# Performance work log

Hardware: AMD Instinct MI355X
Metric: run time of the kernel (lower is better)

The kernel has to match this reference:

```python
import jax, jax.numpy as jnp
import numpy as np
from jax.ops import segment_sum

N_NODES = 50000
N_EDGES = 800000
IN_DIM, HID_DIM, OUT_DIM = 128, 128, 64
N_GRAPHS = 64


def setup_inputs() -> dict:
    key = jax.random.key(0)
    ks = jax.random.split(key, 8)
    x = jax.random.normal(ks[0], (N_NODES, IN_DIM), dtype=jnp.float32)
    edge_index = jax.random.randint(ks[1], (2, N_EDGES), 0, N_NODES, dtype=jnp.int64)
    batch = jnp.sort(jax.random.randint(ks[2], (N_NODES,), 0, N_GRAPHS, dtype=jnp.int64))
    # Glorot-ish init for GCNConv linear weights, zero bias (PyG default)
    W1 = jax.random.normal(ks[3], (IN_DIM, HID_DIM), dtype=jnp.float32) / np.sqrt(IN_DIM)
    b1 = jnp.zeros((HID_DIM,), dtype=jnp.float32)
    W2 = jax.random.normal(ks[4], (HID_DIM, OUT_DIM), dtype=jnp.float32) / np.sqrt(HID_DIM)
    b2 = jnp.zeros((OUT_DIM,), dtype=jnp.float32)
    return {"x": x, "W1": W1, "b1": b1, "W2": W2, "b2": b2,
            "edge_index": edge_index, "batch": batch, "num_graphs": N_GRAPHS}


def _gcn_conv(h, W, b, src, dst, deg_inv_sqrt, n_nodes):
    # h: [N, Fin] -> [N, Fout]; GCNConv: D^{-1/2}(A+I)D^{-1/2} (h W) + b
    hw = h @ W                                   # [N, Fout]
    norm = deg_inv_sqrt[src] * deg_inv_sqrt[dst] # [E]
    msg = hw[src] * norm[:, None]                # [E, Fout] (gather)
    agg = segment_sum(msg, dst, num_segments=n_nodes)  # scatter-add
    # self-loop contribution: norm_ii = deg_inv_sqrt[i]^2
    agg = agg + hw * (deg_inv_sqrt * deg_inv_sqrt)[:, None]
    return agg + b


def reference(x, W1, b1, W2, b2, edge_index, batch, num_graphs):
    n_nodes = x.shape[0]
    src, dst = edge_index[0], edge_index[1]
    # degree of A + I (self-loops added, as in PyG GCNConv default)
    deg = segment_sum(jnp.ones_like(dst, dtype=x.dtype), dst,
                      num_segments=n_nodes) + 1.0
    deg_inv_sqrt = jax.lax.rsqrt(deg)

    h = jax.nn.relu(_gcn_conv(x, W1, b1, src, dst, deg_inv_sqrt, n_nodes))
    h = jax.nn.relu(_gcn_conv(h, W2, b2, src, dst, deg_inv_sqrt, n_nodes))

    # global_mean_pool over batch ids
    sums = segment_sum(h, batch, num_segments=num_graphs)          # [G, Fout]
    counts = segment_sum(jnp.ones((n_nodes,), dtype=h.dtype), batch,
                         num_segments=num_graphs)                  # [G]
    return sums / jnp.maximum(counts, 1.0)[:, None]
```

## Files before the change

kernel.cpp:

```cpp
#include <hip/hip_runtime.h>

typedef float f4 __attribute__((ext_vector_type(4)));
typedef float f2 __attribute__((ext_vector_type(2)));
typedef short s8 __attribute__((ext_vector_type(8)));

union FU { unsigned u[4]; s8 s; };

__device__ __forceinline__ unsigned cvtpk(float lo, float hi){
  unsigned r;
  asm("v_cvt_pk_bf16_f32 %0, %1, %2" : "=v"(r) : "v"(lo), "v"(hi));
  return r;
}

__device__ __forceinline__ float bflo(unsigned v){ return __uint_as_float(v << 16); }
__device__ __forceinline__ float bfhi(unsigned v){ return __uint_as_float(v & 0xFFFF0000u); }

__device__ __forceinline__ int ld_idx(const void* p, int i, int is64){
  if (is64) return (int)((const long long*)p)[i];
  return ((const int*)p)[i];
}

__device__ __forceinline__ int detect64(const unsigned* __restrict__ e_raw, int e){
  int lane = threadIdx.x & 63;
  int lim = (e < 1024) ? e : 1024;
  int nz = 0;
  for (int i = lane; i < lim; i += 64) nz |= (e_raw[2*i + 1] != 0u);
  return (__ballot(nz != 0) == 0ull) ? 1 : 0;
}

template<int NC, int BIN>
__device__ __forceinline__ void gemm_body(const void* __restrict__ Xv,
                                          const float* __restrict__ W,
                                          unsigned short* __restrict__ Yb,
                                          int n, int blk, char* Alds){
  constexpr int NCF = NC/16;
  constexpr int WPC = 8/NCF;
  constexpr int RT  = 8/WPC;
  const int tid  = threadIdx.x;
  const int wave = tid >> 6, lane = tid & 63;
  const int rb = blk * 128;

  const int cbase = (wave % NCF) * 16;
  const int rt0   = (wave / NCF) * RT;
  const int col   = cbase + (lane & 15);
  const int kr0   = (lane >> 4) * 8;
  FU bu[4];
#pragma unroll
  for (int ks = 0; ks < 4; ++ks){
    float wv[8];
#pragma unroll
    for (int j = 0; j < 8; ++j) wv[j] = W[(size_t)(ks*32 + kr0 + j)*NC + col];
#pragma unroll
    for (int q = 0; q < 4; ++q) bu[ks].u[q] = cvtpk(wv[2*q], wv[2*q+1]);
  }

  for (int i = tid; i < 128*32; i += 512){
    int row = i >> 5, kq = i & 31;
    int rsrc = rb + row; if (rsrc >= n) rsrc = n - 1;
    uint2 dw;
    if (BIN){
      dw = ((const uint2*)Xv)[(size_t)rsrc*32 + kq];
    } else {
      f4 xv = ((const f4*)Xv)[(size_t)rsrc*32 + kq];
      dw = make_uint2(cvtpk(xv[0], xv[1]), cvtpk(xv[2], xv[3]));
    }
    int byte = (row*256 + kq*8) ^ ((row & 7) << 4);
    *reinterpret_cast<uint2*>(Alds + byte) = dw;
  }
  __syncthreads();

  f4 acc[RT];
#pragma unroll
  for (int rt = 0; rt < RT; ++rt) acc[rt] = 0.0f;

#pragma unroll
  for (int rt = 0; rt < RT; ++rt){
    const int arow = (rt0 + rt)*16 + (lane & 15);
#pragma unroll
    for (int ks = 0; ks < 4; ++ks){
      int kb = ks*32 + kr0;
      int byte = (arow*256 + kb*2) ^ ((arow & 7) << 4);
      s8 a = *reinterpret_cast<const s8*>(Alds + byte);
      acc[rt] = __builtin_amdgcn_mfma_f32_16x16x32_bf16(a, bu[ks].s, acc[rt], 0, 0, 0);
    }
  }

#pragma unroll
  for (int rt = 0; rt < RT; ++rt){
    int rowb = rb + (rt0 + rt)*16 + 4*(lane >> 4);
#pragma unroll
    for (int r = 0; r < 4; ++r){
      int row = rowb + r;
      if (row < n) Yb[(size_t)row*NC + col] = (unsigned short)cvtpk(acc[rt][r], acc[rt][r]);
    }
  }
}

template<int NC, int BIN>
__global__ __launch_bounds__(512) void gemm_k(const void* __restrict__ X,
                                              const float* __restrict__ W,
                                              unsigned short* __restrict__ Yb, int n){
  __shared__ int4 AldsV[2048];
  gemm_body<NC, BIN>(X, W, Yb, n, blockIdx.x, (char*)AldsV);
}

__global__ __launch_bounds__(512) void fused1_k(const float* __restrict__ X,
                                                const float* __restrict__ W1,
                                                unsigned short* __restrict__ Yb,
                                                const void* __restrict__ eidx,
                                                const void* __restrict__ batchp,
                                                int* __restrict__ counts,
                                                int* __restrict__ batch32,
                                                int n, int e, int GB, int CB){
  __shared__ int4 AldsV[2048];
  __shared__ int hist[512];
  int blk = blockIdx.x;
  if (blk < GB){
    gemm_body<128, 0>(X, W1, Yb, n, blk, (char*)AldsV);
    return;
  }
  blk -= GB;
  const int NBK = (n + 127) >> 7;
  for (int i = threadIdx.x; i < NBK; i += 512) hist[i] = 0;
  __syncthreads();
  int is64 = detect64((const unsigned*)eidx, e);
  int CHK = (e + CB - 1) / CB;
  int beg = blk*CHK, end = min(e, beg + CHK);
  for (int i = beg + (int)threadIdx.x; i < end; i += 512){
    int d = ld_idx(eidx, e + i, is64);
    atomicAdd(&hist[d >> 7], 1);
  }
  __syncthreads();
  for (int i = threadIdx.x; i < NBK; i += 512) counts[i*CB + blk] = hist[i];
  for (int i = blk*512 + (int)threadIdx.x; i < n; i += CB*512)
    batch32[i] = ld_idx(batchp, i, is64);
}

__global__ void scanA_k(const int* __restrict__ counts, int* __restrict__ base,
                        int* __restrict__ bsum, int L){
  __shared__ int sh[256];
  int tid = threadIdx.x;
  int i = blockIdx.x*256 + tid;
  int v = (i < L) ? counts[i] : 0;
  sh[tid] = v; __syncthreads();
  for (int off = 1; off < 256; off <<= 1){
    int t = (tid >= off) ? sh[tid - off] : 0;
    __syncthreads();
    sh[tid] += t;
    __syncthreads();
  }
  if (i < L) base[i] = sh[tid] - v;
  if (tid == 255) bsum[blockIdx.x] = sh[255];
}

__global__ __launch_bounds__(512) void scanB2_k(int* __restrict__ bsum, int nb,
                                                int* __restrict__ rowptr,
                                                float* __restrict__ outsum,
                                                int totalOut, int n, int e){
  __shared__ int sh[512];
  int tid = threadIdx.x;
  int v = (tid < nb) ? bsum[tid] : 0;
  sh[tid] = v; __syncthreads();
  for (int off = 1; off < 512; off <<= 1){
    int t = (tid >= off) ? sh[tid - off] : 0;
    __syncthreads();
    sh[tid] += t;
    __syncthreads();
  }
  if (tid < nb) bsum[tid] = sh[tid] - v;
  if (tid == nb - 1) bsum[nb] = sh[tid];
  if (tid == 0) rowptr[n] = e;
  for (int k = tid; k < totalOut; k += 512) outsum[k] = 0.0f;
}

__global__ __launch_bounds__(512) void scat_k(const void* __restrict__ eidx,
                                              const int* __restrict__ base,
                                              const int* __restrict__ bsum,
                                              int* __restrict__ packed,
                                              int n, int e, int CB){
  __shared__ int cur[512];
  int blk = blockIdx.x, tid = threadIdx.x;
  const int NBK = (n + 127) >> 7;
  for (int i = tid; i < NBK; i += 512) cur[i] = bsum[i] + base[i*CB + blk];
  __syncthreads();
  int is64 = detect64((const unsigned*)eidx, e);
  int CHK = (e + CB - 1) / CB;
  int beg = blk*CHK, end = min(e, beg + CHK);
  for (int i = beg + tid; i < end; i += 512){
    int s = ld_idx(eidx, i, is64);
    int d = ld_idx(eidx, e + i, is64);
    int pos = atomicAdd(&cur[d >> 7], 1);
    packed[pos] = s | ((d & 127) << 16);
  }
}

#define CSR_CAP 6144
__global__ __launch_bounds__(256) void csr_k(const int* __restrict__ packed,
                                             const int* __restrict__ bsum,
                                             int* __restrict__ esrcS,
                                             int* __restrict__ rowptr,
                                             float* __restrict__ dinv, int n){
  __shared__ int vals[CSR_CAP];
  __shared__ int hist[128], off[128], cur[128];
  int b = blockIdx.x, tid = threadIdx.x;
  int sbeg = bsum[b], send = bsum[b + 1];
  int m = send - sbeg;
  int mL = min(m, CSR_CAP);
  for (int i = tid; i < mL; i += 256) vals[i] = packed[sbeg + i];
  if (tid < 128) hist[tid] = 0;
  __syncthreads();
  for (int i = tid; i < m; i += 256){
    int v = (i < CSR_CAP) ? vals[i] : packed[sbeg + i];
    atomicAdd(&hist[(v >> 16) & 127], 1);
  }
  __syncthreads();
  if (tid < 128) off[tid] = hist[tid];
  __syncthreads();
  for (int o = 1; o < 128; o <<= 1){
    int v = 0;
    if (tid < 128 && tid >= o) v = off[tid - o];
    __syncthreads();
    if (tid < 128) off[tid] += v;
    __syncthreads();
  }
  if (tid < 128){
    int ex = off[tid] - hist[tid];
    cur[tid] = ex;
    int node = b*128 + tid;
    if (node < n){
      rowptr[node] = sbeg + ex;
      dinv[node] = rsqrtf((float)hist[tid] + 1.0f);
    }
  }
  __syncthreads();
  for (int i = tid; i < m; i += 256){
    int v = (i < CSR_CAP) ? vals[i] : packed[sbeg + i];
    int pos = atomicAdd(&cur[(v >> 16) & 127], 1);
    esrcS[sbeg + pos] = v & 0xFFFF;
  }
}

template<int NC, int OB>
__global__ __launch_bounds__(256) void agg_k(const unsigned short* __restrict__ HWb,
                                             const float* __restrict__ dinv,
                                             const int* __restrict__ rowptr,
                                             const int* __restrict__ esrcS,
                                             const float* __restrict__ bias,
                                             void* __restrict__ Hout, int n){
  int wid  = (blockIdx.x*256 + threadIdx.x) >> 6;
  int lane = threadIdx.x & 63;
  if (wid >= n) return;
  wid = __builtin_amdgcn_readfirstlane(wid);
  float di = dinv[wid];
  float di2 = di * di;
  int beg = __builtin_amdgcn_readfirstlane(rowptr[wid]);
  int end = __builtin_amdgcn_readfirstlane(rowptr[wid + 1]);
  if (NC == 128){
    unsigned sv = ((const unsigned*)(HWb + (size_t)wid*128))[lane];
    float a0 = bflo(sv) * di2, a1 = bfhi(sv) * di2;
    int j = beg;
    for (; j + 16 <= end; j += 16){
      int s[16]; float dv[16]; unsigned v[16];
#pragma unroll
      for (int t = 0; t < 16; ++t) s[t] = esrcS[j + t];
#pragma unroll
      for (int t = 0; t < 16; ++t){
        dv[t] = dinv[s[t]];
        v[t] = ((const unsigned*)(HWb + (size_t)s[t]*128))[lane];
      }
#pragma unroll
      for (int t = 0; t < 16; ++t){
        float wt = dv[t] * di;
        a0 += bflo(v[t]) * wt;
        a1 += bfhi(v[t]) * wt;
      }
    }
    for (; j + 4 <= end; j += 4){
      int s[4]; float dv[4]; unsigned v[4];
#pragma unroll
      for (int t = 0; t < 4; ++t) s[t] = esrcS[j + t];
#pragma unroll
      for (int t = 0; t < 4; ++t){
        dv[t] = dinv[s[t]];
        v[t] = ((const unsigned*)(HWb + (size_t)s[t]*128))[lane];
      }
#pragma unroll
      for (int t = 0; t < 4; ++t){
        float wt = dv[t] * di;
        a0 += bflo(v[t]) * wt;
        a1 += bfhi(v[t]) * wt;
      }
    }
    for (; j < end; ++j){
      int s = esrcS[j];
      float wt = dinv[s] * di;
      unsigned v = ((const unsigned*)(HWb + (size_t)s*128))[lane];
      a0 += bflo(v) * wt;
      a1 += bfhi(v) * wt;
    }
    f2 bb = ((const f2*)bias)[lane];
    a0 = fmaxf(a0 + bb[0], 0.0f);
    a1 = fmaxf(a1 + bb[1], 0.0f);
    if (OB){
      ((unsigned*)Hout)[(size_t)wid*64 + lane] = cvtpk(a0, a1);
    } else {
      f2 r; r[0] = a0; r[1] = a1;
      ((f2*)Hout)[(size_t)wid*64 + lane] = r;
    }
  } else {
    float acc = bflo((unsigned)HWb[(size_t)wid*64 + lane]) * di2;
    int j = beg;
    for (; j + 16 <= end; j += 16){
      int s[16]; float dv[16]; unsigned v[16];
#pragma unroll
      for (int t = 0; t < 16; ++t) s[t] = esrcS[j + t];
#pragma unroll
      for (int t = 0; t < 16; ++t){
        dv[t] = dinv[s[t]];
        v[t] = (unsigned)HWb[(size_t)s[t]*64 + lane];
      }
#pragma unroll
      for (int t = 0; t < 16; ++t) acc += bflo(v[t]) * (dv[t] * di);
    }
    for (; j + 4 <= end; j += 4){
      int s[4]; float dv[4]; unsigned v[4];
#pragma unroll
      for (int t = 0; t < 4; ++t) s[t] = esrcS[j + t];
#pragma unroll
      for (int t = 0; t < 4; ++t){
        dv[t] = dinv[s[t]];
        v[t] = (unsigned)HWb[(size_t)s[t]*64 + lane];
      }
#pragma unroll
      for (int t = 0; t < 4; ++t) acc += bflo(v[t]) * (dv[t] * di);
    }
    for (; j < end; ++j){
      int s = esrcS[j];
      acc += bflo((unsigned)HWb[(size_t)s*64 + lane]) * (dinv[s] * di);
    }
    acc = fmaxf(acc + bias[lane], 0.0f);
    ((float*)Hout)[(size_t)wid*64 + lane] = acc;
  }
}

__global__ __launch_bounds__(256) void pool_k(const float* __restrict__ H2,
                                              const int* __restrict__ batch32,
                                              float* __restrict__ outsum, int n){
  int wid  = (blockIdx.x*256 + threadIdx.x) >> 6;
  int lane = threadIdx.x & 63;
  int start = wid * 8;
  if (start >= n) return;
  int cnt = min(8, n - start);
  float v[8]; int b[8];
#pragma unroll
  for (int t = 0; t < 8; ++t){
    int i = start + t; if (i >= n) i = n - 1;
    v[t] = H2[(size_t)i*64 + lane];
    b[t] = batch32[i];
  }
  float acc = 0.0f;
  int gcur = b[0];
#pragma unroll
  for (int t = 0; t < 8; ++t){
    if (t < cnt){
      if (b[t] != gcur){
        unsafeAtomicAdd(&outsum[gcur*64 + lane], acc);
        acc = 0.0f; gcur = b[t];
      }
      acc += v[t];
    }
  }
  unsafeAtomicAdd(&outsum[gcur*64 + lane], acc);
}

__global__ void fin_k(const float* __restrict__ outsum,
                      const int* __restrict__ batch32,
                      float* __restrict__ out, int n, int g){
  __shared__ int starts[257];
  int t = threadIdx.x;
  if (t <= g){
    int lo = 0, hi = n;
    while (lo < hi){ int mid = (lo + hi) >> 1; if (batch32[mid] < t) lo = mid + 1; else hi = mid; }
    starts[t] = lo;
  }
  __syncthreads();
  for (int idx = t; idx < (g << 6); idx += 256){
    int gi = idx >> 6;
    float c = (float)(starts[gi + 1] - starts[gi]);
    out[idx] = outsum[idx] / fmaxf(c, 1.0f);
  }
}

extern "C" void kernel_launch(void* const* d_in, const int* in_sizes, int n_in,
                              void* d_out, int out_size, void* d_ws, size_t ws_size,
                              hipStream_t stream){
  const float* x    = (const float*)d_in[0];
  const float* W1   = (const float*)d_in[1];
  const float* b1   = (const float*)d_in[2];
  const float* W2   = (const float*)d_in[3];
  const float* b2   = (const float*)d_in[4];
  const void*  eidx = d_in[5];
  const void*  batchp = d_in[6];
  const int n = in_sizes[0] / 128;
  const int e = in_sizes[5] / 2;
  const int g = out_size / 64;
  float* out = (float*)d_out;

  const int NBK = (n + 127) >> 7;
  const int CB  = 256;
  const int GB  = (n + 127) / 128;
  const int L   = NBK * CB;

  char* w = (char*)d_ws;
  int* counts  = (int*)w;
  int* base    = counts + (size_t)L;
  int* bsum    = base + (size_t)L;
  int* rowptr  = bsum + (NBK + 1);
  int* batch32 = rowptr + (n + 1);
  float* dinv  = (float*)(batch32 + n);
  float* outsum = dinv + n;
  int* packed  = (int*)(outsum + out_size);
  int* esrcS   = packed + e;
  size_t ofs = (size_t)((char*)(esrcS + e) - w);
  ofs = (ofs + 255) & ~(size_t)255;
  unsigned short* HWb = (unsigned short*)(w + ofs);
  size_t ofs2 = ofs + (size_t)n * 128 * 2;
  ofs2 = (ofs2 + 255) & ~(size_t)255;
  unsigned short* Hb = (unsigned short*)(w + ofs2);
  size_t ofs3 = ofs2 + (size_t)n * 128 * 2;
  ofs3 = (ofs3 + 255) & ~(size_t)255;
  float* H2 = (float*)(w + ofs3);

  fused1_k<<<GB + CB, 512, 0, stream>>>(x, W1, HWb, eidx, batchp,
                                        counts, batch32, n, e, GB, CB);
  scanA_k<<<NBK, 256, 0, stream>>>(counts, base, bsum, L);
  scanB2_k<<<1, 512, 0, stream>>>(bsum, NBK, rowptr, outsum, out_size, n, e);
  scat_k<<<CB, 512, 0, stream>>>(eidx, base, bsum, packed, n, e, CB);
  csr_k<<<NBK, 256, 0, stream>>>(packed, bsum, esrcS, rowptr, dinv, n);

  agg_k<128, 1><<<(n + 3)/4, 256, 0, stream>>>(HWb, dinv, rowptr, esrcS, b1, Hb, n);
  gemm_k<64, 1><<<GB, 512, 0, stream>>>(Hb, W2, HWb, n);
  agg_k<64, 0><<<(n + 3)/4, 256, 0, stream>>>(HWb, dinv, rowptr, esrcS, b2, H2, n);

  int pw = (n + 7)/8;
  pool_k<<<(pw + 3)/4, 256, 0, stream>>>(H2, batch32, outsum, n);
  fin_k<<<1, 256, 0, stream>>>(outsum, batch32, out, n, g);
}
```

Measured before the change: 124.1 us.

## Fold scanB into scatter, cache packed edges, fuse pooling into layer-2 aggregation

The histogram kernel now writes a packed edge word (src, low dst bits, dst bucket), so the scatter kernel reads 4 bytes per edge instead of re-reading 64-bit src/dst and re-detecting the index width. The single-block second-level scan is removed: each scatter block redundantly scans the bucket sums, and block 0 publishes them for csr_k. The output zeroing moves into scanA. Layer-2 aggregation now atomically adds into the per-graph sums directly, which drops the H2 buffer and the pool kernel but adds one atomic per node per lane on only 64 graph rows, a contention risk.

```diff
diff --git a/kernel.cpp b/kernel.cpp
--- a/kernel.cpp
+++ b/kernel.cpp
@@ -110,6 +110,7 @@
                                                 const void* __restrict__ eidx,
                                                 const void* __restrict__ batchp,
                                                 int* __restrict__ counts,
+                                                unsigned* __restrict__ etmp,
                                                 int* __restrict__ batch32,
                                                 int n, int e, int GB, int CB){
   __shared__ int4 AldsV[2048];
@@ -127,8 +128,10 @@
   int CHK = (e + CB - 1) / CB;
   int beg = blk*CHK, end = min(e, beg + CHK);
   for (int i = beg + (int)threadIdx.x; i < end; i += 512){
+    int s = ld_idx(eidx, i, is64);
     int d = ld_idx(eidx, e + i, is64);
     atomicAdd(&hist[d >> 7], 1);
+    etmp[i] = (unsigned)s | ((unsigned)(d & 127) << 16) | ((unsigned)(d >> 7) << 23);
   }
   __syncthreads();
   for (int i = threadIdx.x; i < NBK; i += 512) counts[i*CB + blk] = hist[i];
@@ -137,7 +140,8 @@
 }
 
 __global__ void scanA_k(const int* __restrict__ counts, int* __restrict__ base,
-                        int* __restrict__ bsum, int L){
+                        int* __restrict__ bsum, int L,
+                        float* __restrict__ outsum, int totalOut){
   __shared__ int sh[256];
   int tid = threadIdx.x;
   int i = blockIdx.x*256 + tid;
@@ -151,59 +155,56 @@
   }
   if (i < L) base[i] = sh[tid] - v;
   if (tid == 255) bsum[blockIdx.x] = sh[255];
-}
-
-__global__ __launch_bounds__(512) void scanB2_k(int* __restrict__ bsum, int nb,
-                                                int* __restrict__ rowptr,
-                                                float* __restrict__ outsum,
-                                                int totalOut, int n, int e){
-  __shared__ int sh[512];
-  int tid = threadIdx.x;
-  int v = (tid < nb) ? bsum[tid] : 0;
-  sh[tid] = v; __syncthreads();
-  for (int off = 1; off < 512; off <<= 1){
-    int t = (tid >= off) ? sh[tid - off] : 0;
-    __syncthreads();
-    sh[tid] += t;
-    __syncthreads();
-  }
-  if (tid < nb) bsum[tid] = sh[tid] - v;
-  if (tid == nb - 1) bsum[nb] = sh[tid];
-  if (tid == 0) rowptr[n] = e;
-  for (int k = tid; k < totalOut; k += 512) outsum[k] = 0.0f;
-}
-
-__global__ __launch_bounds__(512) void scat_k(const void* __restrict__ eidx,
+  if (blockIdx.x == 0){
+    for (int k = tid; k < totalOut; k += 256) outsum[k] = 0.0f;
+  }
+}
+
+__global__ __launch_bounds__(512) void scat_k(const unsigned* __restrict__ etmp,
                                               const int* __restrict__ base,
                                               const int* __restrict__ bsum,
+                                              int* __restrict__ bsumS,
                                               int* __restrict__ packed,
                                               int n, int e, int CB){
+  __shared__ int sh[512];
   __shared__ int cur[512];
   int blk = blockIdx.x, tid = threadIdx.x;
   const int NBK = (n + 127) >> 7;
-  for (int i = tid; i < NBK; i += 512) cur[i] = bsum[i] + base[i*CB + blk];
-  __syncthreads();
-  int is64 = detect64((const unsigned*)eidx, e);
+  int v = (tid < NBK) ? bsum[tid] : 0;
+  sh[tid] = v; __syncthreads();
+  for (int o = 1; o < 512; o <<= 1){
+    int t = (tid >= o) ? sh[tid - o] : 0;
+    __syncthreads();
+    sh[tid] += t;
+    __syncthreads();
+  }
+  int ex = sh[tid] - v;
+  if (tid < NBK) cur[tid] = ex + base[tid*CB + blk];
+  if (blk == 0){
+    if (tid < NBK) bsumS[tid] = ex;
+    if (tid == NBK - 1) bsumS[NBK] = sh[tid];
+  }
+  __syncthreads();
   int CHK = (e + CB - 1) / CB;
   int beg = blk*CHK, end = min(e, beg + CHK);
   for (int i = beg + tid; i < end; i += 512){
-    int s = ld_idx(eidx, i, is64);
-    int d = ld_idx(eidx, e + i, is64);
-    int pos = atomicAdd(&cur[d >> 7], 1);
-    packed[pos] = s | ((d & 127) << 16);
+    unsigned w = etmp[i];
+    int pos = atomicAdd(&cur[w >> 23], 1);
+    packed[pos] = (int)(w & 0x7FFFFFu);
   }
 }
 
 #define CSR_CAP 6144
 __global__ __launch_bounds__(256) void csr_k(const int* __restrict__ packed,
-                                             const int* __restrict__ bsum,
+                                             const int* __restrict__ bsumS,
                                              int* __restrict__ esrcS,
                                              int* __restrict__ rowptr,
-                                             float* __restrict__ dinv, int n){
+                                             float* __restrict__ dinv, int n, int e){
   __shared__ int vals[CSR_CAP];
   __shared__ int hist[128], off[128], cur[128];
   int b = blockIdx.x, tid = threadIdx.x;
-  int sbeg = bsum[b], send = bsum[b + 1];
+  if (b == 0 && tid == 0) rowptr[n] = e;
+  int sbeg = bsumS[b], send = bsumS[b + 1];
   int m = send - sbeg;
   int mL = min(m, CSR_CAP);
   for (int i = tid; i < mL; i += 256) vals[i] = packed[sbeg + i];
@@ -240,13 +241,12 @@
   }
 }
 
-template<int NC, int OB>
-__global__ __launch_bounds__(256) void agg_k(const unsigned short* __restrict__ HWb,
-                                             const float* __restrict__ dinv,
-                                             const int* __restrict__ rowptr,
-                                             const int* __restrict__ esrcS,
-                                             const float* __restrict__ bias,
-                                             void* __restrict__ Hout, int n){
+__global__ __launch_bounds__(256) void agg128_k(const unsigned short* __restrict__ HWb,
+                                                const float* __restrict__ dinv,
+                                                const int* __restrict__ rowptr,
+                                                const int* __restrict__ esrcS,
+                                                const float* __restrict__ bias,
+                                                unsigned* __restrict__ Hb, int n){
   int wid  = (blockIdx.x*256 + threadIdx.x) >> 6;
   int lane = threadIdx.x & 63;
   if (wid >= n) return;
@@ -255,122 +255,102 @@
   float di2 = di * di;
   int beg = __builtin_amdgcn_readfirstlane(rowptr[wid]);
   int end = __builtin_amdgcn_readfirstlane(rowptr[wid + 1]);
-  if (NC == 128){
-    unsigned sv = ((const unsigned*)(HWb + (size_t)wid*128))[lane];
-    float a0 = bflo(sv) * di2, a1 = bfhi(sv) * di2;
-    int j = beg;
-    for (; j + 16 <= end; j += 16){
-      int s[16]; float dv[16]; unsigned v[16];
-#pragma unroll
-      for (int t = 0; t < 16; ++t) s[t] = esrcS[j + t];
-#pragma unroll
-      for (int t = 0; t < 16; ++t){
-        dv[t] = dinv[s[t]];
-        v[t] = ((const unsigned*)(HWb + (size_t)s[t]*128))[lane];
-      }
-#pragma unroll
-      for (int t = 0; t < 16; ++t){
-        float wt = dv[t] * di;
-        a0 += bflo(v[t]) * wt;
-        a1 += bfhi(v[t]) * wt;
-      }
-    }
-    for (; j + 4 <= end; j += 4){
-      int s[4]; float dv[4]; unsigned v[4];
-#pragma unroll
-      for (int t = 0; t < 4; ++t) s[t] = esrcS[j + t];
-#pragma unroll
-      for (int t = 0; t < 4; ++t){
-        dv[t] = dinv[s[t]];
-        v[t] = ((const unsigned*)(HWb + (size_t)s[t]*128))[lane];
-      }
-#pragma unroll
-      for (int t = 0; t < 4; ++t){
-        float wt = dv[t] * di;
-        a0 += bflo(v[t]) * wt;
-        a1 += bfhi(v[t]) * wt;
-      }
-    }
-    for (; j < end; ++j){
-      int s = esrcS[j];
-      float wt = dinv[s] * di;
-      unsigned v = ((const unsigned*)(HWb + (size_t)s*128))[lane];
-      a0 += bflo(v) * wt;
-      a1 += bfhi(v) * wt;
-    }
-    f2 bb = ((const f2*)bias)[lane];
-    a0 = fmaxf(a0 + bb[0], 0.0f);
-    a1 = fmaxf(a1 + bb[1], 0.0f);
-    if (OB){
-      ((unsigned*)Hout)[(size_t)wid*64 + lane] = cvtpk(a0, a1);
-    } else {
-      f2 r; r[0] = a0; r[1] = a1;
-      ((f2*)Hout)[(size_t)wid*64 + lane] = r;
-    }
-  } else {
-    float acc = bflo((unsigned)HWb[(size_t)wid*64 + lane]) * di2;
-    int j = beg;
-    for (; j + 16 <= end; j += 16){
-      int s[16]; float dv[16]; unsigned v[16];
-#pragma unroll
-      for (int t = 0; t < 16; ++t) s[t] = esrcS[j + t];
-#pragma unroll
-      for (int t = 0; t < 16; ++t){
-        dv[t] = dinv[s[t]];
-        v[t] = (unsigned)HWb[(size_t)s[t]*64 + lane];
-      }
-#pragma unroll
-      for (int t = 0; t < 16; ++t) acc += bflo(v[t]) * (dv[t] * di);
-    }
-    for (; j + 4 <= end; j += 4){
-      int s[4]; float dv[4]; unsigned v[4];
-#pragma unroll
-      for (int t = 0; t < 4; ++t) s[t] = esrcS[j + t];
-#pragma unroll
-      for (int t = 0; t < 4; ++t){
-        dv[t] = dinv[s[t]];
-        v[t] = (unsigned)HWb[(size_t)s[t]*64 + lane];
-      }
-#pragma unroll
-      for (int t = 0; t < 4; ++t) acc += bflo(v[t]) * (dv[t] * di);
-    }
-    for (; j < end; ++j){
-      int s = esrcS[j];
-      acc += bflo((unsigned)HWb[(size_t)s*64 + lane]) * (dinv[s] * di);
-    }
-    acc = fmaxf(acc + bias[lane], 0.0f);
-    ((float*)Hout)[(size_t)wid*64 + lane] = acc;
-  }
-}
-
-__global__ __launch_bounds__(256) void pool_k(const float* __restrict__ H2,
-                                              const int* __restrict__ batch32,
-                                              float* __restrict__ outsum, int n){
+  unsigned sv = ((const unsigned*)(HWb + (size_t)wid*128))[lane];
+  float a0 = bflo(sv) * di2, a1 = bfhi(sv) * di2;
+  int j = beg;
+  for (; j + 16 <= end; j += 16){
+    int s[16]; float dv[16]; unsigned v[16];
+#pragma unroll
+    for (int t = 0; t < 16; ++t) s[t] = esrcS[j + t];
+#pragma unroll
+    for (int t = 0; t < 16; ++t){
+      dv[t] = dinv[s[t]];
+      v[t] = ((const unsigned*)(HWb + (size_t)s[t]*128))[lane];
+    }
+#pragma unroll
+    for (int t = 0; t < 16; ++t){
+      float wt = dv[t] * di;
+      a0 += bflo(v[t]) * wt;
+      a1 += bfhi(v[t]) * wt;
+    }
+  }
+  for (; j + 4 <= end; j += 4){
+    int s[4]; float dv[4]; unsigned v[4];
+#pragma unroll
+    for (int t = 0; t < 4; ++t) s[t] = esrcS[j + t];
+#pragma unroll
+    for (int t = 0; t < 4; ++t){
+      dv[t] = dinv[s[t]];
+      v[t] = ((const unsigned*)(HWb + (size_t)s[t]*128))[lane];
+    }
+#pragma unroll
+    for (int t = 0; t < 4; ++t){
+      float wt = dv[t] * di;
+      a0 += bflo(v[t]) * wt;
+      a1 += bfhi(v[t]) * wt;
+    }
+  }
+  for (; j < end; ++j){
+    int s = esrcS[j];
+    float wt = dinv[s] * di;
+    unsigned v = ((const unsigned*)(HWb + (size_t)s*128))[lane];
+    a0 += bflo(v) * wt;
+    a1 += bfhi(v) * wt;
+  }
+  f2 bb = ((const f2*)bias)[lane];
+  a0 = fmaxf(a0 + bb[0], 0.0f);
+  a1 = fmaxf(a1 + bb[1], 0.0f);
+  Hb[(size_t)wid*64 + lane] = cvtpk(a0, a1);
+}
+
+__global__ __launch_bounds__(256) void agg64p_k(const unsigned short* __restrict__ HWb,
+                                                const float* __restrict__ dinv,
+                                                const int* __restrict__ rowptr,
+                                                const int* __restrict__ esrcS,
+                                                const float* __restrict__ bias,
+                                                const int* __restrict__ batch32,
+                                                float* __restrict__ outsum, int n){
   int wid  = (blockIdx.x*256 + threadIdx.x) >> 6;
   int lane = threadIdx.x & 63;
-  int start = wid * 8;
-  if (start >= n) return;
-  int cnt = min(8, n - start);
-  float v[8]; int b[8];
-#pragma unroll
-  for (int t = 0; t < 8; ++t){
-    int i = start + t; if (i >= n) i = n - 1;
-    v[t] = H2[(size_t)i*64 + lane];
-    b[t] = batch32[i];
-  }
-  float acc = 0.0f;
-  int gcur = b[0];
-#pragma unroll
-  for (int t = 0; t < 8; ++t){
-    if (t < cnt){
-      if (b[t] != gcur){
-        unsafeAtomicAdd(&outsum[gcur*64 + lane], acc);
-        acc = 0.0f; gcur = b[t];
-      }
-      acc += v[t];
-    }
-  }
-  unsafeAtomicAdd(&outsum[gcur*64 + lane], acc);
+  if (wid >= n) return;
+  wid = __builtin_amdgcn_readfirstlane(wid);
+  float di = dinv[wid];
+  float di2 = di * di;
+  int beg = __builtin_amdgcn_readfirstlane(rowptr[wid]);
+  int end = __builtin_amdgcn_readfirstlane(rowptr[wid + 1]);
+  float acc = bflo((unsigned)HWb[(size_t)wid*64 + lane]) * di2;
+  int j = beg;
+  for (; j + 16 <= end; j += 16){
+    int s[16]; float dv[16]; unsigned v[16];
+#pragma unroll
+    for (int t = 0; t < 16; ++t) s[t] = esrcS[j + t];
+#pragma unroll
+    for (int t = 0; t < 16; ++t){
+      dv[t] = dinv[s[t]];
+      v[t] = (unsigned)HWb[(size_t)s[t]*64 + lane];
+    }
+#pragma unroll
+    for (int t = 0; t < 16; ++t) acc += bflo(v[t]) * (dv[t] * di);
+  }
+  for (; j + 4 <= end; j += 4){
+    int s[4]; float dv[4]; unsigned v[4];
+#pragma unroll
+    for (int t = 0; t < 4; ++t) s[t] = esrcS[j + t];
+#pragma unroll
+    for (int t = 0; t < 4; ++t){
+      dv[t] = dinv[s[t]];
+      v[t] = (unsigned)HWb[(size_t)s[t]*64 + lane];
+    }
+#pragma unroll
+    for (int t = 0; t < 4; ++t) acc += bflo(v[t]) * (dv[t] * di);
+  }
+  for (; j < end; ++j){
+    int s = esrcS[j];
+    acc += bflo((unsigned)HWb[(size_t)s*64 + lane]) * (dinv[s] * di);
+  }
+  acc = fmaxf(acc + bias[lane], 0.0f);
+  int gid = batch32[wid];
+  unsafeAtomicAdd(&outsum[gid*64 + lane], acc);
 }
 
 __global__ void fin_k(const float* __restrict__ outsum,
@@ -415,11 +395,13 @@
   int* counts  = (int*)w;
   int* base    = counts + (size_t)L;
   int* bsum    = base + (size_t)L;
-  int* rowptr  = bsum + (NBK + 1);
+  int* bsumS   = bsum + NBK;
+  int* rowptr  = bsumS + (NBK + 1);
   int* batch32 = rowptr + (n + 1);
   float* dinv  = (float*)(batch32 + n);
   float* outsum = dinv + n;
-  int* packed  = (int*)(outsum + out_size);
+  unsigned* etmp = (unsigned*)(outsum + out_size);
+  int* packed  = (int*)(etmp + e);
   int* esrcS   = packed + e;
   size_t ofs = (size_t)((char*)(esrcS + e) - w);
   ofs = (ofs + 255) & ~(size_t)255;
@@ -427,22 +409,17 @@
   size_t ofs2 = ofs + (size_t)n * 128 * 2;
   ofs2 = (ofs2 + 255) & ~(size_t)255;
   unsigned short* Hb = (unsigned short*)(w + ofs2);
-  size_t ofs3 = ofs2 + (size_t)n * 128 * 2;
-  ofs3 = (ofs3 + 255) & ~(size_t)255;
-  float* H2 = (float*)(w + ofs3);
 
   fused1_k<<<GB + CB, 512, 0, stream>>>(x, W1, HWb, eidx, batchp,
-                                        counts, batch32, n, e, GB, CB);
-  scanA_k<<<NBK, 256, 0, stream>>>(counts, base, bsum, L);
-  scanB2_k<<<1, 512, 0, stream>>>(bsum, NBK, rowptr, outsum, out_size, n, e);
-  scat_k<<<CB, 512, 0, stream>>>(eidx, base, bsum, packed, n, e, CB);
-  csr_k<<<NBK, 256, 0, stream>>>(packed, bsum, esrcS, rowptr, dinv, n);
-
-  agg_k<128, 1><<<(n + 3)/4, 256, 0, stream>>>(HWb, dinv, rowptr, esrcS, b1, Hb, n);
+                                        counts, etmp, batch32, n, e, GB, CB);
+  scanA_k<<<NBK, 256, 0, stream>>>(counts, base, bsum, L, outsum, out_size);
+  scat_k<<<CB, 512, 0, stream>>>(etmp, base, bsum, bsumS, packed, n, e, CB);
+  csr_k<<<NBK, 256, 0, stream>>>(packed, bsumS, esrcS, rowptr, dinv, n, e);
+
+  agg128_k<<<(n + 3)/4, 256, 0, stream>>>(HWb, dinv, rowptr, esrcS, b1,
+                                          (unsigned*)Hb, n);
   gemm_k<64, 1><<<GB, 512, 0, stream>>>(Hb, W2, HWb, n);
-  agg_k<64, 0><<<(n + 3)/4, 256, 0, stream>>>(HWb, dinv, rowptr, esrcS, b2, H2, n);
-
-  int pw = (n + 7)/8;
-  pool_k<<<(pw + 3)/4, 256, 0, stream>>>(H2, batch32, outsum, n);
+  agg64p_k<<<(n + 3)/4, 256, 0, stream>>>(HWb, dinv, rowptr, esrcS, b2,
+                                          batch32, outsum, n);
   fin_k<<<1, 256, 0, stream>>>(outsum, batch32, out, n, g);
 }
```

New measurement: 161.8 us. +30.3%, slower.
